# Optimization experiments

Measured on AMD Instinct MI355X. Metric: run time of the kernel, lower is better.

## Reference

```python
import jax, jax.numpy as jnp
import numpy as np

EPS = 1e-12  # F.normalize default eps


def _sage_conv(x, src, dst, num_nodes, W_l, W_r, b):
    # mean-aggregate neighbor features: for each dst node, mean over x[src]
    agg = jax.ops.segment_sum(x[src], dst, num_segments=num_nodes)  # [N, d_in]
    cnt = jax.ops.segment_sum(jnp.ones((src.shape[0],), x.dtype), dst,
                              num_segments=num_nodes)
    mean = agg / jnp.maximum(cnt, 1.0)[:, None]
    # PyG SAGEConv: lin_l(aggregated) + bias + lin_r(root)
    return mean @ W_l + b + x @ W_r


def setup_inputs() -> dict:
    key = jax.random.key(0)
    ks = jax.random.split(key, 10)
    N, E, F_in = 50000, 400000, 128
    x = jax.random.normal(ks[0], (N, F_in), dtype=jnp.float32)
    edge_index = jax.random.randint(ks[1], (2, E), 0, N, dtype=jnp.int64)

    def lin(k, din, dout):
        s = 1.0 / np.sqrt(din)
        return jax.random.uniform(k, (din, dout), jnp.float32, -s, s)

    params = {
        "W1_l": lin(ks[2], F_in, 2048), "W1_r": lin(ks[3], F_in, 2048),
        "b1": jnp.zeros((2048,), jnp.float32),
        "W2_l": lin(ks[4], 2048, 2048), "W2_r": lin(ks[5], 2048, 2048),
        "b2": jnp.zeros((2048,), jnp.float32),
        "W3_l": lin(ks[6], 2048, 1024), "W3_r": lin(ks[7], 2048, 1024),
        "b3": jnp.zeros((1024,), jnp.float32),
    }
    return {"x": x, "unused": 0, "edge_index": edge_index, **params}


def reference(x, unused, edge_index,
              W1_l, W1_r, b1, W2_l, W2_r, b2, W3_l, W3_r, b3):
    del unused
    N = x.shape[0]
    src, dst = edge_index[0], edge_index[1]
    h = jax.nn.relu(_sage_conv(x, src, dst, N, W1_l, W1_r, b1))
    h = jax.nn.relu(_sage_conv(h, src, dst, N, W2_l, W2_r, b2))
    h = jax.nn.relu(_sage_conv(h, src, dst, N, W3_l, W3_r, b3))
    # F.normalize(dim=1): x / max(||x||_2, eps)
    norm = jnp.linalg.norm(h, axis=1, keepdims=True)
    return h / jnp.maximum(norm, EPS)
```

## Files before the change

### kernel.cpp

```cpp
#include <hip/hip_runtime.h>
#include <stdint.h>

#define NN 50000
#define EE 400000

typedef unsigned short u16;
typedef __attribute__((ext_vector_type(8))) short bf16x8;
typedef __attribute__((ext_vector_type(4))) float f32x4;
typedef __attribute__((address_space(3))) uint32_t lds_u32_t;
typedef __attribute__((address_space(1))) uint32_t glob_u32_t;

__device__ inline float bf2f(u16 u) {
  union { uint32_t i; float f; } x; x.i = ((uint32_t)u) << 16; return x.f;
}
__device__ inline u16 f2bf(float f) {
  union { float f; uint32_t i; } x; x.f = f;
  x.i += 0x7fffu + ((x.i >> 16) & 1u);
  return (u16)(x.i >> 16);
}
__device__ inline void gload_lds16(const void* g, void* l) {
  __builtin_amdgcn_global_load_lds((const glob_u32_t*)g, (lds_u32_t*)l, 16, 0, 0);
}

__global__ void detect_i64(const int* __restrict__ e, int* __restrict__ flag) {
  __shared__ int sh[256];
  int t = threadIdx.x;
  int v = 0;
  for (int i = t; i < 4096; i += 256) v |= e[2 * i + 1];
  sh[t] = v; __syncthreads();
  for (int s = 128; s > 0; s >>= 1) { if (t < s) sh[t] |= sh[t + s]; __syncthreads(); }
  if (t == 0) flag[0] = (sh[0] == 0) ? 1 : 0;
}

__global__ void conv_edges(const int* __restrict__ e, const int* __restrict__ flag,
                           int* __restrict__ src, int* __restrict__ dst) {
  int i = blockIdx.x * 256 + threadIdx.x;
  if (i >= EE) return;
  if (flag[0]) { src[i] = e[2 * i]; dst[i] = e[2 * (EE + i)]; }
  else         { src[i] = e[i];     dst[i] = e[EE + i]; }
}

__global__ void count_edges(const int* __restrict__ dst, int* __restrict__ cnt) {
  int i = blockIdx.x * 256 + threadIdx.x;
  if (i < EE) atomicAdd(&cnt[dst[i]], 1);
}

__global__ void scan_counts(const int* __restrict__ cnt, int* __restrict__ offs,
                            int* __restrict__ cursor) {
  __shared__ int sh[1024];
  __shared__ int carry_sh;
  int tid = threadIdx.x;
  if (tid == 0) carry_sh = 0;
  __syncthreads();
  int nChunks = (NN + 1023) / 1024;
  for (int c = 0; c < nChunks; ++c) {
    int idx = c * 1024 + tid;
    int v = (idx < NN) ? cnt[idx] : 0;
    sh[tid] = v; __syncthreads();
    for (int off = 1; off < 1024; off <<= 1) {
      int t = (tid >= off) ? sh[tid - off] : 0;
      __syncthreads();
      sh[tid] += t;
      __syncthreads();
    }
    int incl = sh[tid];
    int excl = incl - v + carry_sh;
    if (idx < NN) { offs[idx] = excl; cursor[idx] = excl; }
    __syncthreads();
    if (tid == 0) carry_sh += sh[1023];
    __syncthreads();
  }
}

__global__ void fill_buckets(const int* __restrict__ src, const int* __restrict__ dst,
                             int* __restrict__ cursor, int* __restrict__ bucket) {
  int i = blockIdx.x * 256 + threadIdx.x;
  if (i >= EE) return;
  int p = atomicAdd(&cursor[dst[i]], 1);
  bucket[p] = src[i];
}

__global__ void cvt_bf16(const float* __restrict__ in, u16* __restrict__ out, int n4) {
  int i = blockIdx.x * 256 + threadIdx.x;
  if (i >= n4) return;
  float4 v = ((const float4*)in)[i];
  u16 o[4] = { f2bf(v.x), f2bf(v.y), f2bf(v.z), f2bf(v.w) };
  uint2 pack;
  pack.x = (uint32_t)o[0] | ((uint32_t)o[1] << 16);
  pack.y = (uint32_t)o[2] | ((uint32_t)o[3] << 16);
  ((uint2*)out)[i] = pack;
}

__global__ void transposeW(const float* __restrict__ W, u16* __restrict__ Wt,
                           int K, int Nc) {
  __shared__ float tile[32][33];
  int n0 = blockIdx.x * 32, k0 = blockIdx.y * 32;
  int tx = threadIdx.x, ty = threadIdx.y;
  #pragma unroll
  for (int i = 0; i < 4; ++i)
    tile[ty + i * 8][tx] = W[(size_t)(k0 + ty + i * 8) * Nc + n0 + tx];
  __syncthreads();
  #pragma unroll
  for (int i = 0; i < 4; ++i)
    Wt[(size_t)(n0 + ty + i * 8) * K + k0 + tx] = f2bf(tile[tx][ty + i * 8]);
}

template<int D>
__global__ void agg_mean(const u16* __restrict__ h, const int* __restrict__ offs,
                         const int* __restrict__ cnt, const int* __restrict__ bucket,
                         u16* __restrict__ outp) {
  int node = blockIdx.x;
  int t = threadIdx.x;
  int base = t * 8;
  if (base >= D) return;
  int start = offs[node];
  int c = cnt[node];
  float acc[8];
  #pragma unroll
  for (int i = 0; i < 8; ++i) acc[i] = 0.f;
  for (int j = 0; j < c; ++j) {
    int s = bucket[start + j];
    uint4 q = *(const uint4*)(h + (size_t)s * D + base);
    acc[0] += bf2f((u16)(q.x & 0xffff)); acc[1] += bf2f((u16)(q.x >> 16));
    acc[2] += bf2f((u16)(q.y & 0xffff)); acc[3] += bf2f((u16)(q.y >> 16));
    acc[4] += bf2f((u16)(q.z & 0xffff)); acc[5] += bf2f((u16)(q.z >> 16));
    acc[6] += bf2f((u16)(q.w & 0xffff)); acc[7] += bf2f((u16)(q.w >> 16));
  }
  float inv = 1.0f / fmaxf((float)c, 1.0f);
  uint4 o;
  o.x = (uint32_t)f2bf(acc[0] * inv) | ((uint32_t)f2bf(acc[1] * inv) << 16);
  o.y = (uint32_t)f2bf(acc[2] * inv) | ((uint32_t)f2bf(acc[3] * inv) << 16);
  o.z = (uint32_t)f2bf(acc[4] * inv) | ((uint32_t)f2bf(acc[5] * inv) << 16);
  o.w = (uint32_t)f2bf(acc[6] * inv) | ((uint32_t)f2bf(acc[7] * inv) << 16);
  *(uint4*)(outp + (size_t)node * D + base) = o;
}

__global__ void agg_add_norm(const u16* __restrict__ Y, const int* __restrict__ offs,
                             const int* __restrict__ cnt, const int* __restrict__ bucket,
                             const float* __restrict__ b3, float* __restrict__ outp) {
  int node = blockIdx.x;
  int t = threadIdx.x;
  int base = t * 4;
  int start = offs[node];
  int c = cnt[node];
  float acc[4] = {0.f, 0.f, 0.f, 0.f};
  for (int j = 0; j < c; ++j) {
    int s = bucket[start + j];
    uint2 q = *(const uint2*)(Y + (size_t)s * 2048 + base);
    acc[0] += bf2f((u16)(q.x & 0xffff)); acc[1] += bf2f((u16)(q.x >> 16));
    acc[2] += bf2f((u16)(q.y & 0xffff)); acc[3] += bf2f((u16)(q.y >> 16));
  }
  float inv = 1.0f / fmaxf((float)c, 1.0f);
  uint2 qr = *(const uint2*)(Y + (size_t)node * 2048 + 1024 + base);
  float yr[4] = { bf2f((u16)(qr.x & 0xffff)), bf2f((u16)(qr.x >> 16)),
                  bf2f((u16)(qr.y & 0xffff)), bf2f((u16)(qr.y >> 16)) };
  float4 bv = *(const float4*)(b3 + base);
  float v[4];
  v[0] = fmaxf(acc[0] * inv + yr[0] + bv.x, 0.f);
  v[1] = fmaxf(acc[1] * inv + yr[1] + bv.y, 0.f);
  v[2] = fmaxf(acc[2] * inv + yr[2] + bv.z, 0.f);
  v[3] = fmaxf(acc[3] * inv + yr[3] + bv.w, 0.f);
  float ss = v[0] * v[0] + v[1] * v[1] + v[2] * v[2] + v[3] * v[3];
  #pragma unroll
  for (int off = 32; off > 0; off >>= 1) ss += __shfl_down(ss, off);
  __shared__ float sw[4];
  int lane = t & 63, w = t >> 6;
  if (lane == 0) sw[w] = ss;
  __syncthreads();
  float total = sw[0] + sw[1] + sw[2] + sw[3];
  float scale = 1.0f / fmaxf(sqrtf(total), 1e-12f);
  float4 o = { v[0] * scale, v[1] * scale, v[2] * scale, v[3] * scale };
  *(float4*)(outp + (size_t)node * 1024 + base) = o;
}


template<int K>
__device__ inline void stage_half(char* ldsX, const u16* __restrict__ G, int grow0,
                                  int k0, int h, int wave, int lrow8, int slot8,
                                  int clampR) {
  #pragma unroll
  for (int j = 0; j < 2; ++j) {
    const int lrow = h * 128 + j * 64 + wave * 8;
    int gr = grow0 + lrow + lrow8;
    gr = gr < clampR ? gr : clampR - 1;
    gload_lds16(G + (size_t)gr * K + k0 + slot8, ldsX + lrow * 128);
  }
}

#define LOAD_A(MH)                                                              \
  _Pragma("unroll") for (int mf = 0; mf < 4; ++mf) {                            \
    af[mf][0] = *(const bf16x8*)(cA + ((MH) * 128 + mf * 16) * 128 + kc0);      \
    af[mf][1] = *(const bf16x8*)(cA + ((MH) * 128 + mf * 16) * 128 + kc1);      \
  }
#define LOAD_B(DST, NH)                                                         \
  _Pragma("unroll") for (int nf = 0; nf < 2; ++nf) {                            \
    DST[nf][0] = *(const bf16x8*)(cB + ((NH) * 128 + nf * 16) * 128 + kc0);     \
    DST[nf][1] = *(const bf16x8*)(cB + ((NH) * 128 + nf * 16) * 128 + kc1);     \
  }
#define QUAD(MH, BREG, NH)                                                      \
  _Pragma("unroll") for (int mf = 0; mf < 4; ++mf)                              \
  _Pragma("unroll") for (int nf = 0; nf < 2; ++nf) {                            \
    acc[(MH)*4+mf][(NH)*2+nf] = __builtin_amdgcn_mfma_f32_16x16x32_bf16(        \
        af[mf][0], BREG[nf][0], acc[(MH)*4+mf][(NH)*2+nf], 0, 0, 0);            \
    acc[(MH)*4+mf][(NH)*2+nf] = __builtin_amdgcn_mfma_f32_16x16x32_bf16(        \
        af[mf][1], BREG[nf][1], acc[(MH)*4+mf][(NH)*2+nf], 0, 0, 0);            \
  }

template<int K, bool DUAL, bool EPI, bool OUT_F32>
__global__ __launch_bounds__(512, 2)
void gemm2src(const u16* __restrict__ A1, const u16* __restrict__ A2,
              const u16* __restrict__ B1t, const u16* __restrict__ B2t,
              const float* __restrict__ bias, void* __restrict__ Cout,
              int M, int Nc, int tilesN) {
  __shared__ __align__(16) char lds[131072];
  constexpr int NTp = K / 64;
  constexpr int NT = DUAL ? 2 * NTp : NTp;

  const int nwg = gridDim.x;
  const int bid = blockIdx.x;
  const int wg = (bid & 7) * (nwg >> 3) + (bid >> 3);
  const int bx = wg % tilesN, by = wg / tilesN;
  const int rowBase = by * 256, colBase = bx * 256;

  const int tid = threadIdx.x;
  const int lane = tid & 63;
  const int wave = tid >> 6;
  const int wm = wave >> 2, wn = wave & 3;
  const int r = lane & 15, kg = lane >> 4;
  const int sw = (r & 7) << 4;
  const int kc0 = (kg * 16) ^ sw;
  const int kc1 = (64 + kg * 16) ^ sw;
  const int slot8 = ((lane & 7) ^ ((lane >> 3) & 7)) * 8;
  const int lrow8 = lane >> 3;

  char* const pA0 = lds + (wm * 64 + r) * 128;
  char* const pB0 = lds + 32768 + (wn * 32 + r) * 128;

  f32x4 acc[8][4];
  #pragma unroll
  for (int m = 0; m < 8; ++m)
    #pragma unroll
    for (int n = 0; n < 4; ++n) acc[m][n] = (f32x4){0.f, 0.f, 0.f, 0.f};

  bf16x8 af[4][2], b0[2][2], b1[2][2];

  stage_half<K>(lds,         A1,  rowBase, 0, 0, wave, lrow8, slot8, M);
  stage_half<K>(lds + 32768, B1t, colBase, 0, 0, wave, lrow8, slot8, Nc);
  stage_half<K>(lds + 32768, B1t, colBase, 0, 1, wave, lrow8, slot8, Nc);
  stage_half<K>(lds,         A1,  rowBase, 0, 1, wave, lrow8, slot8, M);
  asm volatile("s_waitcnt vmcnt(0)" ::: "memory");
  __builtin_amdgcn_s_barrier();

  for (int t = 0; t < NT; ++t) {
    const int cur = t & 1;
    const char* cA = pA0 + cur * 65536;
    const char* cB = pB0 + cur * 65536;
    char* nA = lds + (cur ^ 1) * 65536;
    char* nB = nA + 32768;
    const int vt = (t + 1 < NT) ? t + 1 : NT - 1;
    const u16* sA; const u16* sB; int sk0;
    if (DUAL && vt >= NTp) { sA = A2; sB = B2t; sk0 = (vt - NTp) * 64; }
    else                   { sA = A1; sB = B1t; sk0 = vt * 64; }

    stage_half<K>(nA, sA, rowBase, sk0, 0, wave, lrow8, slot8, M);
    stage_half<K>(nB, sB, colBase, sk0, 0, wave, lrow8, slot8, Nc);
    stage_half<K>(nB, sB, colBase, sk0, 1, wave, lrow8, slot8, Nc);
    stage_half<K>(nA, sA, rowBase, sk0, 1, wave, lrow8, slot8, M);

    LOAD_A(0); LOAD_B(b0, 0);
    QUAD(0, b0, 0);
    LOAD_B(b1, 1);
    QUAD(0, b1, 1);
    LOAD_A(1);
    QUAD(1, b1, 1);
    QUAD(1, b0, 0);

    asm volatile("s_waitcnt vmcnt(0)" ::: "memory");
    __builtin_amdgcn_s_barrier();
  }

  const int q = lane >> 4;
  #pragma unroll
  for (int m = 0; m < 8; ++m) {
    int row = rowBase + (m >> 2) * 128 + wm * 64 + (m & 3) * 16 + q * 4;
    #pragma unroll
    for (int n = 0; n < 4; ++n) {
      int col = colBase + (n >> 1) * 128 + wn * 32 + (n & 1) * 16 + r;
      float bv = EPI ? bias[col] : 0.f;
      #pragma unroll
      for (int reg = 0; reg < 4; ++reg) {
        if (row + reg < M) {
          float v = acc[m][n][reg];
          if constexpr (EPI) v = fmaxf(v + bv, 0.f);
          if constexpr (OUT_F32)
            ((float*)Cout)[(size_t)(row + reg) * Nc + col] = v;
          else
            ((u16*)Cout)[(size_t)(row + reg) * Nc + col] = f2bf(v);
        }
      }
    }
  }
}

extern "C" void kernel_launch(void* const* d_in, const int* in_sizes, int n_in,
                              void* d_out, int out_size, void* d_ws, size_t ws_size,
                              hipStream_t stream) {
  const float* x   = (const float*)d_in[0];
  const int*   eix = (const int*)d_in[2];
  const float* W1l = (const float*)d_in[3];
  const float* W1r = (const float*)d_in[4];
  const float* b1  = (const float*)d_in[5];
  const float* W2l = (const float*)d_in[6];
  const float* W2r = (const float*)d_in[7];
  const float* b2  = (const float*)d_in[8];
  const float* W3l = (const float*)d_in[9];
  const float* W3r = (const float*)d_in[10];
  const float* b3  = (const float*)d_in[11];

  char* ws = (char*)d_ws;
  size_t off = 0;
  auto alloc = [&](size_t bytes) -> char* {
    char* p = ws + off;
    off += (bytes + 255) & ~(size_t)255;
    return p;
  };
  int* flag   = (int*)alloc(4);
  int* srcA   = (int*)alloc((size_t)EE * 4);
  int* dstA   = (int*)alloc((size_t)EE * 4);
  int* bucket = (int*)alloc((size_t)EE * 4);
  int* cnt    = (int*)alloc((size_t)NN * 4);
  int* offs   = (int*)alloc((size_t)NN * 4);
  int* cursor = (int*)alloc((size_t)NN * 4);
  u16* xb     = (u16*)alloc((size_t)NN * 128 * 2);
  u16* mean1  = (u16*)alloc((size_t)NN * 128 * 2);
  u16* W1lT   = (u16*)alloc((size_t)2048 * 128 * 2);
  u16* W1rT   = (u16*)alloc((size_t)2048 * 128 * 2);
  u16* W2lT   = (u16*)alloc((size_t)2048 * 2048 * 2);
  u16* W2rT   = (u16*)alloc((size_t)2048 * 2048 * 2);
  u16* W3lT   = (u16*)alloc((size_t)1024 * 2048 * 2);
  u16* W3rT   = (u16*)alloc((size_t)1024 * 2048 * 2);
  u16* bufA   = (u16*)alloc((size_t)NN * 2048 * 2);
  u16* bufB   = (u16*)alloc((size_t)NN * 2048 * 2);
  u16* mean2  = (u16*)d_out;

  detect_i64<<<1, 256, 0, stream>>>(eix, flag);
  conv_edges<<<(EE + 255) / 256, 256, 0, stream>>>(eix, flag, srcA, dstA);

  hipMemsetAsync(cnt, 0, (size_t)NN * 4, stream);
  count_edges<<<(EE + 255) / 256, 256, 0, stream>>>(dstA, cnt);
  scan_counts<<<1, 1024, 0, stream>>>(cnt, offs, cursor);
  fill_buckets<<<(EE + 255) / 256, 256, 0, stream>>>(srcA, dstA, cursor, bucket);

  cvt_bf16<<<(NN * 128 / 4 + 255) / 256, 256, 0, stream>>>(x, xb, NN * 128 / 4);
  transposeW<<<dim3(2048 / 32, 128 / 32), dim3(32, 8), 0, stream>>>(W1l, W1lT, 128, 2048);
  transposeW<<<dim3(2048 / 32, 128 / 32), dim3(32, 8), 0, stream>>>(W1r, W1rT, 128, 2048);
  transposeW<<<dim3(2048 / 32, 2048 / 32), dim3(32, 8), 0, stream>>>(W2l, W2lT, 2048, 2048);
  transposeW<<<dim3(2048 / 32, 2048 / 32), dim3(32, 8), 0, stream>>>(W2r, W2rT, 2048, 2048);
  transposeW<<<dim3(1024 / 32, 2048 / 32), dim3(32, 8), 0, stream>>>(W3l, W3lT, 2048, 1024);
  transposeW<<<dim3(1024 / 32, 2048 / 32), dim3(32, 8), 0, stream>>>(W3r, W3rT, 2048, 1024);

  const int tilesM = (NN + 255) / 256;

  agg_mean<128><<<NN, 64, 0, stream>>>(xb, offs, cnt, bucket, mean1);
  gemm2src<128, true, true, false><<<tilesM * 8, 512, 0, stream>>>(
      mean1, xb, W1lT, W1rT, b1, bufA, NN, 2048, 8);

  agg_mean<2048><<<NN, 256, 0, stream>>>(bufA, offs, cnt, bucket, mean2);
  gemm2src<2048, true, true, false><<<tilesM * 8, 512, 0, stream>>>(
      mean2, bufA, W2lT, W2rT, b2, bufB, NN, 2048, 8);

  gemm2src<2048, false, false, false><<<tilesM * 8, 512, 0, stream>>>(
      bufB, nullptr, W3lT, nullptr, nullptr, bufA, NN, 2048, 8);
  agg_add_norm<<<NN, 256, 0, stream>>>(bufA, offs, cnt, bucket, b3, (float*)d_out);
}
```

Baseline: 2.094 ms.

## Load GEMM B operand directly from global into registers, halve LDS

```diff
diff --git a/kernel.cpp b/kernel.cpp
--- a/kernel.cpp
+++ b/kernel.cpp
@@ -175,9 +175,9 @@
 
 
 template<int K>
-__device__ inline void stage_half(char* ldsX, const u16* __restrict__ G, int grow0,
-                                  int k0, int h, int wave, int lrow8, int slot8,
-                                  int clampR) {
+__device__ inline void stage_halfA(char* ldsX, const u16* __restrict__ G, int grow0,
+                                   int k0, int h, int wave, int lrow8, int slot8,
+                                   int clampR) {
   #pragma unroll
   for (int j = 0; j < 2; ++j) {
     const int lrow = h * 128 + j * 64 + wave * 8;
@@ -192,27 +192,51 @@
     af[mf][0] = *(const bf16x8*)(cA + ((MH) * 128 + mf * 16) * 128 + kc0);      \
     af[mf][1] = *(const bf16x8*)(cA + ((MH) * 128 + mf * 16) * 128 + kc1);      \
   }
-#define LOAD_B(DST, NH)                                                         \
-  _Pragma("unroll") for (int nf = 0; nf < 2; ++nf) {                            \
-    DST[nf][0] = *(const bf16x8*)(cB + ((NH) * 128 + nf * 16) * 128 + kc0);     \
-    DST[nf][1] = *(const bf16x8*)(cB + ((NH) * 128 + nf * 16) * 128 + kc1);     \
-  }
-#define QUAD(MH, BREG, NH)                                                      \
+#define GLOADB(SET, BT, K0)                                                     \
+  _Pragma("unroll") for (int n4 = 0; n4 < 4; ++n4) {                            \
+    const u16* bp = (BT) + (size_t)(colBq + (n4 >> 1) * 128 + (n4 & 1) * 16) * K \
+                    + (K0) + kgE;                                               \
+    SET[n4][0] = *(const bf16x8*)(bp);                                          \
+    SET[n4][1] = *(const bf16x8*)(bp + 32);                                     \
+  }
+#define QUAD(MH, SET, NH)                                                       \
   _Pragma("unroll") for (int mf = 0; mf < 4; ++mf)                              \
   _Pragma("unroll") for (int nf = 0; nf < 2; ++nf) {                            \
     acc[(MH)*4+mf][(NH)*2+nf] = __builtin_amdgcn_mfma_f32_16x16x32_bf16(        \
-        af[mf][0], BREG[nf][0], acc[(MH)*4+mf][(NH)*2+nf], 0, 0, 0);            \
+        af[mf][0], SET[(NH)*2+nf][0], acc[(MH)*4+mf][(NH)*2+nf], 0, 0, 0);      \
     acc[(MH)*4+mf][(NH)*2+nf] = __builtin_amdgcn_mfma_f32_16x16x32_bf16(        \
-        af[mf][1], BREG[nf][1], acc[(MH)*4+mf][(NH)*2+nf], 0, 0, 0);            \
+        af[mf][1], SET[(NH)*2+nf][1], acc[(MH)*4+mf][(NH)*2+nf], 0, 0, 0);      \
+  }
+
+#define TILE_BODY(t, CURSET, NXTSET)                                            \
+  {                                                                             \
+    const int cur = (t) & 1;                                                    \
+    const char* cA = pA0 + cur * 32768;                                         \
+    char* nA = lds + (cur ^ 1) * 32768;                                         \
+    const int vt = ((t) + 1 < NT) ? (t) + 1 : NT - 1;                           \
+    const u16* sA; const u16* sB; int sk0;                                      \
+    if (DUAL && vt >= NTp) { sA = A2; sB = B2t; sk0 = (vt - NTp) * 64; }        \
+    else                   { sA = A1; sB = B1t; sk0 = vt * 64; }                \
+    stage_halfA<K>(nA, sA, rowBase, sk0, 0, wave, lrow8, slot8, M);             \
+    stage_halfA<K>(nA, sA, rowBase, sk0, 1, wave, lrow8, slot8, M);             \
+    GLOADB(NXTSET, sB, sk0);                                                    \
+    LOAD_A(0);                                                                  \
+    QUAD(0, CURSET, 0);                                                         \
+    QUAD(0, CURSET, 1);                                                         \
+    LOAD_A(1);                                                                  \
+    QUAD(1, CURSET, 1);                                                         \
+    QUAD(1, CURSET, 0);                                                         \
+    asm volatile("s_waitcnt vmcnt(8)" ::: "memory");                            \
+    __builtin_amdgcn_s_barrier();                                               \
   }
 
 template<int K, bool DUAL, bool EPI, bool OUT_F32>
 __global__ __launch_bounds__(512, 2)
-void gemm2src(const u16* __restrict__ A1, const u16* __restrict__ A2,
-              const u16* __restrict__ B1t, const u16* __restrict__ B2t,
-              const float* __restrict__ bias, void* __restrict__ Cout,
-              int M, int Nc, int tilesN) {
-  __shared__ __align__(16) char lds[131072];
+void gemmBD(const u16* __restrict__ A1, const u16* __restrict__ A2,
+            const u16* __restrict__ B1t, const u16* __restrict__ B2t,
+            const float* __restrict__ bias, void* __restrict__ Cout,
+            int M, int Nc, int tilesN) {
+  __shared__ __align__(16) char lds[65536];
   constexpr int NTp = K / 64;
   constexpr int NT = DUAL ? 2 * NTp : NTp;
 
@@ -232,9 +256,10 @@
   const int kc1 = (64 + kg * 16) ^ sw;
   const int slot8 = ((lane & 7) ^ ((lane >> 3) & 7)) * 8;
   const int lrow8 = lane >> 3;
+  const int colBq = colBase + wn * 32 + r;
+  const int kgE = kg * 8;
 
   char* const pA0 = lds + (wm * 64 + r) * 128;
-  char* const pB0 = lds + 32768 + (wn * 32 + r) * 128;
 
   f32x4 acc[8][4];
   #pragma unroll
@@ -242,42 +267,21 @@
     #pragma unroll
     for (int n = 0; n < 4; ++n) acc[m][n] = (f32x4){0.f, 0.f, 0.f, 0.f};
 
-  bf16x8 af[4][2], b0[2][2], b1[2][2];
-
-  stage_half<K>(lds,         A1,  rowBase, 0, 0, wave, lrow8, slot8, M);
-  stage_half<K>(lds + 32768, B1t, colBase, 0, 0, wave, lrow8, slot8, Nc);
-  stage_half<K>(lds + 32768, B1t, colBase, 0, 1, wave, lrow8, slot8, Nc);
-  stage_half<K>(lds,         A1,  rowBase, 0, 1, wave, lrow8, slot8, M);
+  bf16x8 af[4][2], bX[4][2], bY[4][2];
+
+  stage_halfA<K>(lds, A1, rowBase, 0, 0, wave, lrow8, slot8, M);
+  stage_halfA<K>(lds, A1, rowBase, 0, 1, wave, lrow8, slot8, M);
+  GLOADB(bX, B1t, 0);
+  asm volatile("s_waitcnt vmcnt(8)" ::: "memory");
+  __builtin_amdgcn_s_barrier();
+
+  #pragma unroll 1
+  for (int t = 0; t < NT; t += 2) {
+    TILE_BODY(t,     bX, bY);
+    TILE_BODY(t + 1, bY, bX);
+  }
+
   asm volatile("s_waitcnt vmcnt(0)" ::: "memory");
-  __builtin_amdgcn_s_barrier();
-
-  for (int t = 0; t < NT; ++t) {
-    const int cur = t & 1;
-    const char* cA = pA0 + cur * 65536;
-    const char* cB = pB0 + cur * 65536;
-    char* nA = lds + (cur ^ 1) * 65536;
-    char* nB = nA + 32768;
-    const int vt = (t + 1 < NT) ? t + 1 : NT - 1;
-    const u16* sA; const u16* sB; int sk0;
-    if (DUAL && vt >= NTp) { sA = A2; sB = B2t; sk0 = (vt - NTp) * 64; }
-    else                   { sA = A1; sB = B1t; sk0 = vt * 64; }
-
-    stage_half<K>(nA, sA, rowBase, sk0, 0, wave, lrow8, slot8, M);
-    stage_half<K>(nB, sB, colBase, sk0, 0, wave, lrow8, slot8, Nc);
-    stage_half<K>(nB, sB, colBase, sk0, 1, wave, lrow8, slot8, Nc);
-    stage_half<K>(nA, sA, rowBase, sk0, 1, wave, lrow8, slot8, M);
-
-    LOAD_A(0); LOAD_B(b0, 0);
-    QUAD(0, b0, 0);
-    LOAD_B(b1, 1);
-    QUAD(0, b1, 1);
-    LOAD_A(1);
-    QUAD(1, b1, 1);
-    QUAD(1, b0, 0);
-
-    asm volatile("s_waitcnt vmcnt(0)" ::: "memory");
-    __builtin_amdgcn_s_barrier();
-  }
 
   const int q = lane >> 4;
   #pragma unroll
@@ -362,14 +366,14 @@
   const int tilesM = (NN + 255) / 256;
 
   agg_mean<128><<<NN, 64, 0, stream>>>(xb, offs, cnt, bucket, mean1);
-  gemm2src<128, true, true, false><<<tilesM * 8, 512, 0, stream>>>(
+  gemmBD<128, true, true, false><<<tilesM * 8, 512, 0, stream>>>(
       mean1, xb, W1lT, W1rT, b1, bufA, NN, 2048, 8);
 
   agg_mean<2048><<<NN, 256, 0, stream>>>(bufA, offs, cnt, bucket, mean2);
-  gemm2src<2048, true, true, false><<<tilesM * 8, 512, 0, stream>>>(
+  gemmBD<2048, true, true, false><<<tilesM * 8, 512, 0, stream>>>(
       mean2, bufA, W2lT, W2rT, b2, bufB, NN, 2048, 8);
 
-  gemm2src<2048, false, false, false><<<tilesM * 8, 512, 0, stream>>>(
+  gemmBD<2048, false, false, false><<<tilesM * 8, 512, 0, stream>>>(
       bufB, nullptr, W3lT, nullptr, nullptr, bufA, NN, 2048, 8);
   agg_add_norm<<<NN, 256, 0, stream>>>(bufA, offs, cnt, bucket, b3, (float*)d_out);
 }
```

Result: slower. 2.568 ms (+22.6%).
